# Kernel tuning notes

Measured on AMD Instinct MI355X. Metric: run time of the kernel, lower is better.

The kernel has to match this reference:

```python
import jax, jax.numpy as jnp
import numpy as np


def setup_inputs() -> dict:
    key = jax.random.key(0)
    ks = jax.random.split(key, 5)
    B, S, D = 2, 2048, 1024
    inv = 1.0 / np.sqrt(D)
    inp = {
        "x": jax.random.normal(ks[0], (B, S, D), jnp.float32),
        "Wq": jax.random.normal(ks[1], (D, D), jnp.float32) * inv,
        "bq": jnp.zeros((D,), jnp.float32),
        "Wk": jax.random.normal(ks[2], (D, D), jnp.float32) * inv,
        "bk": jnp.zeros((D,), jnp.float32),
        "Wv": jax.random.normal(ks[3], (D, D), jnp.float32) * inv,
        "bv": jnp.zeros((D,), jnp.float32),
        "Wo": jax.random.normal(ks[4], (D, D), jnp.float32) * inv,
        "bo": jnp.zeros((D,), jnp.float32),
        "num_heads": 16,
        "window_size": 128,
    }
    return inp


def reference(x, Wq, bq, Wk, bk, Wv, bv, Wo, bo, num_heads, window_size):
    B, S, D = x.shape
    H = num_heads
    hd = D // H
    scale = 1.0 / np.sqrt(hd)

    def split_heads(t):  # [B,S,D] -> [B,H,S,hd]
        return t.reshape(B, S, H, hd).transpose(0, 2, 1, 3)

    q = split_heads(x @ Wq + bq)
    k = split_heads(x @ Wk + bk)
    v = split_heads(x @ Wv + bv)

    # dense scores, then sliding-window + causal mask (faithful to original)
    scores = jnp.einsum('bhqd,bhkd->bhqk', q, k) * scale  # [B,H,S,S]
    i = jnp.arange(S)[:, None]
    j = jnp.arange(S)[None, :]
    # position i attends to j in [i - window_size + 1, i]
    mask = (j <= i) & (j > i - window_size)
    scores = jnp.where(mask, scores, -jnp.inf)
    attn_weights = jax.nn.softmax(scores, axis=-1)  # dropout is identity in eval

    out = jnp.einsum('bhqk,bhkd->bhqd', attn_weights, v)  # [B,H,S,hd]
    out = out.transpose(0, 2, 1, 3).reshape(B, S, D)
    return out @ Wo + bo, attn_weights
```

## Files before the change

kernel.cpp:

```cpp
#include <hip/hip_runtime.h>
#include <cmath>

typedef __attribute__((ext_vector_type(8))) __bf16 v8bf;
typedef __attribute__((ext_vector_type(4))) float  v4f;

#define DEV static __device__ __forceinline__

DEV unsigned short f2bf(float f) {
  unsigned u = __builtin_bit_cast(unsigned, f);
  unsigned r = u + 0x7fffu + ((u >> 16) & 1u);
  return (unsigned short)(r >> 16);
}
DEV float bf2f(unsigned short s) {
  return __builtin_bit_cast(float, ((unsigned)s) << 16);
}
DEV v8bf ld8(const unsigned short* p) { return *(const v8bf*)p; }

DEV void gl16(const unsigned short* g, unsigned short* l) {
  __builtin_amdgcn_global_load_lds(
      (const __attribute__((address_space(1))) unsigned int*)g,
      (__attribute__((address_space(3))) unsigned int*)l, 16, 0, 0);
}

__global__ __launch_bounds__(256) void k_prep(const float* __restrict__ x,
                                              const float* __restrict__ Wq,
                                              const float* __restrict__ Wk,
                                              const float* __restrict__ Wv,
                                              const float* __restrict__ Wo,
                                              const float* __restrict__ bq,
                                              const float* __restrict__ bk,
                                              const float* __restrict__ bv,
                                              unsigned short* __restrict__ xb,
                                              unsigned short* __restrict__ WT,
                                              unsigned short* __restrict__ WoT,
                                              float* __restrict__ bqkv) {
  __shared__ float t[32][33];
  int bx = blockIdx.x, tid = threadIdx.x;
  if (bx < 4096) {
    int i = bx * 256 + tid;
    float4 v = ((const float4*)x)[i];
    unsigned lo = (unsigned)f2bf(v.x) | ((unsigned)f2bf(v.y) << 16);
    unsigned hi = (unsigned)f2bf(v.z) | ((unsigned)f2bf(v.w) << 16);
    ((uint2*)xb)[i] = make_uint2(lo, hi);
  } else if (bx < 8192) {
    int rem = bx - 4096;
    int z = rem >> 10, r2 = rem & 1023;
    const float* src = (z == 0) ? Wq : (z == 1) ? Wk : (z == 2) ? Wv : Wo;
    unsigned short* dst = (z < 3) ? WT + z * 1048576 : WoT;
    int n0 = (r2 & 31) * 32, k0 = (r2 >> 5) * 32;
    int tx = tid & 31, ty = tid >> 5;
    for (int r = ty; r < 32; r += 8)
      t[r][tx] = src[(k0 + r) * 1024 + n0 + tx];
    __syncthreads();
    for (int r = ty; r < 32; r += 8)
      dst[(n0 + r) * 1024 + k0 + tx] = f2bf(t[tx][r]);
  } else {
    int i = (bx - 8192) * 256 + tid;
    float v = (i < 1024) ? bq[i] : (i < 2048 ? bk[i - 1024] : bv[i - 2048]);
    bqkv[i] = v;
  }
}

__global__ __launch_bounds__(256) void k_gemm1(const unsigned short* __restrict__ A,
                                               const unsigned short* __restrict__ Bt,
                                               const float* __restrict__ bias,
                                               unsigned short* __restrict__ Cout,
                                               unsigned short* __restrict__ Vtg) {
  constexpr int K = 1024;
  __shared__ __attribute__((aligned(16))) unsigned short As[128 * 32];
  __shared__ __attribute__((aligned(16))) unsigned short Bs[128 * 32];
  int tid = threadIdx.x;
  int wave = tid >> 6, lane = tid & 63;
  int m0 = blockIdx.y * 128, n0 = blockIdx.x * 128;
  int wm = (wave >> 1) * 64, wn = (wave & 1) * 64;
  int m = lane & 15, q4 = lane >> 4;
  int arow = tid >> 2, acol = (tid & 3) * 8;
  v4f acc[4][4] = {};
  const unsigned short* ga0 = A + (m0 + arow) * K + acol;
  const unsigned short* ga1 = A + (m0 + 64 + arow) * K + acol;
  const unsigned short* gb0 = Bt + (n0 + arow) * K + acol;
  const unsigned short* gb1 = Bt + (n0 + 64 + arow) * K + acol;
  unsigned short* lA0 = As + wave * 512;
  unsigned short* lA1 = As + 2048 + wave * 512;
  unsigned short* lB0 = Bs + wave * 512;
  unsigned short* lB1 = Bs + 2048 + wave * 512;

  for (int kt = 0; kt < K; kt += 32) {
    gl16(ga0 + kt, lA0);
    gl16(ga1 + kt, lA1);
    gl16(gb0 + kt, lB0);
    gl16(gb1 + kt, lB1);
    __syncthreads();
    v8bf af[4], bfv[4];
#pragma unroll
    for (int mt = 0; mt < 4; mt++) af[mt] = ld8(&As[(wm + mt * 16 + m) * 32 + q4 * 8]);
#pragma unroll
    for (int nt = 0; nt < 4; nt++) bfv[nt] = ld8(&Bs[(wn + nt * 16 + m) * 32 + q4 * 8]);
#pragma unroll
    for (int mt = 0; mt < 4; mt++)
#pragma unroll
      for (int nt = 0; nt < 4; nt++)
        acc[mt][nt] = __builtin_amdgcn_mfma_f32_16x16x32_bf16(af[mt], bfv[nt], acc[mt][nt], 0, 0, 0);
    __syncthreads();
  }
  if (n0 < 2048) {
#pragma unroll
    for (int mt = 0; mt < 4; mt++)
#pragma unroll
      for (int nt = 0; nt < 4; nt++) {
        int col = n0 + wn + nt * 16 + m;
        float bb = bias[col];
#pragma unroll
        for (int r = 0; r < 4; r++) {
          int row = m0 + wm + mt * 16 + q4 * 4 + r;
          Cout[row * 3072 + col] = f2bf(acc[mt][nt][r] + bb);
        }
      }
  } else {
    int b = m0 >> 11;
#pragma unroll
    for (int mt = 0; mt < 4; mt++)
#pragma unroll
      for (int nt = 0; nt < 4; nt++) {
        int col = n0 + wn + nt * 16 + m;
        float bb = bias[col];
        int dfull = col - 2048;
        int s = (m0 & 2047) + wm + mt * 16 + q4 * 4;
        unsigned short e0 = f2bf(acc[mt][nt][0] + bb);
        unsigned short e1 = f2bf(acc[mt][nt][1] + bb);
        unsigned short e2 = f2bf(acc[mt][nt][2] + bb);
        unsigned short e3 = f2bf(acc[mt][nt][3] + bb);
        uint2 pk = make_uint2((unsigned)e0 | ((unsigned)e1 << 16),
                              (unsigned)e2 | ((unsigned)e3 << 16));
        *(uint2*)&Vtg[((size_t)(b * 1024 + dfull)) * 2048 + s] = pk;
      }
  }
}

__global__ __launch_bounds__(256, 4) void k_attn(const unsigned short* __restrict__ QKV,
                                                 const unsigned short* __restrict__ Vtg,
                                                 unsigned short* __restrict__ Oatt,
                                                 unsigned short* __restrict__ cb) {
  constexpr int PSS = 168;
  __shared__ __attribute__((aligned(16))) unsigned short Ps[4][16 * PSS];
  int b = blockIdx.z, h = blockIdx.y, i0 = blockIdx.x * 64;
  int tid = threadIdx.x, wave = tid >> 6, lane = tid & 63;
  int kbase = i0 - 128;
  const int ld = 3072;
  const unsigned short* Qg = QKV + b * 2048 * ld + h * 64;
  const unsigned short* Kg = Qg + 1024;
  const unsigned short* vsrc = Vtg + (size_t)(b * 16 + h) * 64 * 2048;

  for (int c = lane; c < 16 * 24; c += 64)
    Ps[wave][(c / 24) * PSS + 144 + (c % 24)] = 0;

  int qb = i0 + wave * 16;
  int m = lane & 15, q4 = lane >> 4;

  const unsigned short* qrow = Qg + (qb + m) * ld;
  v8bf qa0 = ld8(qrow + q4 * 8);
  v8bf qa1 = ld8(qrow + 32 + q4 * 8);

  v4f sc[9];
#pragma unroll
  for (int n = 0; n < 9; n++) {
    int key = kbase + wave * 16 + n * 16 + m;
    int kg = key < 0 ? 0 : key;
    const unsigned short* krow = Kg + kg * ld;
    v8bf kb0 = ld8(krow + q4 * 8);
    v8bf kb1 = ld8(krow + 32 + q4 * 8);
    v4f z = {0.f, 0.f, 0.f, 0.f};
    z = __builtin_amdgcn_mfma_f32_16x16x32_bf16(qa0, kb0, z, 0, 0, 0);
    z = __builtin_amdgcn_mfma_f32_16x16x32_bf16(qa1, kb1, z, 0, 0, 0);
    sc[n] = z;
  }
  float mx[4] = {-3e38f, -3e38f, -3e38f, -3e38f};
#pragma unroll
  for (int n = 0; n < 9; n++)
#pragma unroll
    for (int r = 0; r < 4; r++) {
      int i = qb + q4 * 4 + r;
      int j = kbase + wave * 16 + n * 16 + m;
      float v = sc[n][r] * 0.125f;
      bool ok = (j >= 0) && (j <= i) && (j > i - 128);
      v = ok ? v : -3e38f;
      sc[n][r] = v;
      mx[r] = fmaxf(mx[r], v);
    }
#pragma unroll
  for (int o = 1; o < 16; o <<= 1)
#pragma unroll
    for (int r = 0; r < 4; r++) mx[r] = fmaxf(mx[r], __shfl_xor(mx[r], o, 64));
  float sum[4] = {0.f, 0.f, 0.f, 0.f};
#pragma unroll
  for (int n = 0; n < 9; n++)
#pragma unroll
    for (int r = 0; r < 4; r++) {
      float p = __expf(sc[n][r] - mx[r]);
      sc[n][r] = p;
      sum[r] += p;
    }
#pragma unroll
  for (int o = 1; o < 16; o <<= 1)
#pragma unroll
    for (int r = 0; r < 4; r++) sum[r] += __shfl_xor(sum[r], o, 64);
  float inv[4];
#pragma unroll
  for (int r = 0; r < 4; r++) inv[r] = 1.0f / sum[r];

#pragma unroll
  for (int n = 0; n < 9; n++)
#pragma unroll
    for (int r = 0; r < 4; r++)
      Ps[wave][(q4 * 4 + r) * PSS + n * 16 + m] = f2bf(sc[n][r] * inv[r]);

  v4f oacc[4] = {};
#pragma unroll
  for (int c = 0; c < 5; c++) {
    v8bf pa = ld8(&Ps[wave][m * PSS + c * 32 + q4 * 8]);
    int vcol = kbase + wave * 16 + c * 32 + q4 * 8;
    vcol = vcol < 0 ? 0 : (vcol > 2040 ? 2040 : vcol);
#pragma unroll
    for (int dt = 0; dt < 4; dt++) {
      v8bf vb = ld8(vsrc + (size_t)(dt * 16 + m) * 2048 + vcol);
      oacc[dt] = __builtin_amdgcn_mfma_f32_16x16x32_bf16(pa, vb, oacc[dt], 0, 0, 0);
    }
  }
#pragma unroll
  for (int dt = 0; dt < 4; dt++)
#pragma unroll
    for (int r = 0; r < 4; r++)
      Oatt[(b * 2048 + qb + q4 * 4 + r) * 1024 + h * 64 + dt * 16 + m] = f2bf(oacc[dt][r]);

  for (int R = 0; R < 16; R++) {
    int row = (b * 16 + h) * 2048 + qb + R;
    unsigned short p0 = Ps[wave][R * PSS + R + 1 + lane * 2];
    unsigned short p1 = Ps[wave][R * PSS + R + 2 + lane * 2];
    ((unsigned*)cb)[row * 64 + lane] = (unsigned)p0 | ((unsigned)p1 << 16);
  }
}

__global__ __launch_bounds__(256) void k_tail(const unsigned short* __restrict__ Oat,
                                              const unsigned short* __restrict__ WoT,
                                              const float* __restrict__ bo,
                                              float* __restrict__ out,
                                              const unsigned short* __restrict__ cb,
                                              float* __restrict__ wout) {
  __shared__ __attribute__((aligned(16))) unsigned short As[128 * 32];
  __shared__ __attribute__((aligned(16))) unsigned short Bs[128 * 32];
  int tid = threadIdx.x, wave = tid >> 6, lane = tid & 63;

  if (blockIdx.x < 256) {
    constexpr int K = 1024;
    int bx = blockIdx.x;
    int n0 = (bx & 7) * 128, m0 = (bx >> 3) * 128;
    int wm = (wave >> 1) * 64, wn = (wave & 1) * 64;
    int m = lane & 15, q4 = lane >> 4;
    int arow = tid >> 2, acol = (tid & 3) * 8;
    v4f acc[4][4] = {};
    const unsigned short* ga0 = Oat + (m0 + arow) * K + acol;
    const unsigned short* ga1 = Oat + (m0 + 64 + arow) * K + acol;
    const unsigned short* gb0 = WoT + (n0 + arow) * K + acol;
    const unsigned short* gb1 = WoT + (n0 + 64 + arow) * K + acol;
    unsigned short* lA0 = As + wave * 512;
    unsigned short* lA1 = As + 2048 + wave * 512;
    unsigned short* lB0 = Bs + wave * 512;
    unsigned short* lB1 = Bs + 2048 + wave * 512;
    for (int kt = 0; kt < K; kt += 32) {
      gl16(ga0 + kt, lA0);
      gl16(ga1 + kt, lA1);
      gl16(gb0 + kt, lB0);
      gl16(gb1 + kt, lB1);
      __syncthreads();
      v8bf af[4], bfv[4];
#pragma unroll
      for (int mt = 0; mt < 4; mt++) af[mt] = ld8(&As[(wm + mt * 16 + m) * 32 + q4 * 8]);
#pragma unroll
      for (int nt = 0; nt < 4; nt++) bfv[nt] = ld8(&Bs[(wn + nt * 16 + m) * 32 + q4 * 8]);
#pragma unroll
      for (int mt = 0; mt < 4; mt++)
#pragma unroll
        for (int nt = 0; nt < 4; nt++)
          acc[mt][nt] = __builtin_amdgcn_mfma_f32_16x16x32_bf16(af[mt], bfv[nt], acc[mt][nt], 0, 0, 0);
      __syncthreads();
    }
#pragma unroll
    for (int mt = 0; mt < 4; mt++)
#pragma unroll
      for (int nt = 0; nt < 4; nt++) {
        int col = n0 + wn + nt * 16 + m;
        float bb = bo[col];
#pragma unroll
        for (int r = 0; r < 4; r++) {
          int row = m0 + wm + mt * 16 + q4 * 4 + r;
          out[row * 1024 + col] = acc[mt][nt][r] + bb;
        }
      }
  } else {
    int wb = blockIdx.x - 256;
    int rbase = wb * 16 + wave * 4;
    for (int rr = 0; rr < 4; rr++) {
      int row = rbase + rr;
      int i = row & 2047;
      float* rowp = wout + (size_t)row * 2048;
      const unsigned short* crow = cb + (size_t)row * 128;
      int lo = i - 127;
#pragma unroll
      for (int it = 0; it < 8; it++) {
        int col = it * 256 + lane * 4;
        v4f v = {0.f, 0.f, 0.f, 0.f};
        if (col <= i && col + 3 >= lo) {
#pragma unroll
          for (int e = 0; e < 4; e++) {
            int j = col + e;
            if (j >= lo && j <= i && j >= 0)
              v[e] = bf2f(crow[j - lo]);
          }
        }
        __builtin_nontemporal_store(v, (v4f*)(rowp + col));
      }
    }
  }
}

extern "C" void kernel_launch(void* const* d_in, const int* in_sizes, int n_in,
                              void* d_out, int out_size, void* d_ws, size_t ws_size,
                              hipStream_t stream) {
  (void)in_sizes; (void)n_in; (void)out_size; (void)ws_size;
  const float* x  = (const float*)d_in[0];
  const float* Wq = (const float*)d_in[1];
  const float* bq = (const float*)d_in[2];
  const float* Wk = (const float*)d_in[3];
  const float* bk = (const float*)d_in[4];
  const float* Wv = (const float*)d_in[5];
  const float* bv = (const float*)d_in[6];
  const float* Wo = (const float*)d_in[7];
  const float* bo = (const float*)d_in[8];

  char* ws = (char*)d_ws;
  unsigned short* xb   = (unsigned short*)(ws);
  unsigned short* WT   = (unsigned short*)(ws + 8388608);
  unsigned short* WoT  = (unsigned short*)(ws + 14680064);
  float*          bqkv = (float*)(ws + 16777216);
  unsigned short* QKV  = (unsigned short*)(ws + 16789504);
  unsigned short* Oat  = (unsigned short*)(ws + 41955328);
  unsigned short* cb   = (unsigned short*)(ws + 50343936);
  unsigned short* Vtg  = (unsigned short*)(ws + 67121152);

  float* out  = (float*)d_out;
  float* wout = out + 4194304;

  k_prep<<<8204, 256, 0, stream>>>(x, Wq, Wk, Wv, Wo, bq, bk, bv, xb, WT, WoT, bqkv);
  k_gemm1<<<dim3(24, 32), 256, 0, stream>>>(xb, WT, bqkv, QKV, Vtg);
  k_attn<<<dim3(32, 16, 2), 256, 0, stream>>>(QKV, Vtg, Oat, cb);
  k_tail<<<4352, 256, 0, stream>>>(Oat, WoT, bo, out, cb, wout);
}
```

Measured before the change: 650.2 us.

## Overlap attention-weight zero fill with GEMM and attention kernels

After: 662.8 us. No clear change (+1.9%).

```diff
diff --git a/kernel.cpp b/kernel.cpp
--- a/kernel.cpp
+++ b/kernel.cpp
@@ -65,13 +65,23 @@
                                                const unsigned short* __restrict__ Bt,
                                                const float* __restrict__ bias,
                                                unsigned short* __restrict__ Cout,
-                                               unsigned short* __restrict__ Vtg) {
+                                               unsigned short* __restrict__ Vtg,
+                                               float* __restrict__ wout) {
+  int bx = blockIdx.x, tid = threadIdx.x;
+  if (bx % 3 != 0) {
+    int z = bx - bx / 3 - 1;
+    v4f zv = {0.f, 0.f, 0.f, 0.f};
+    v4f* w4 = (v4f*)wout;
+    for (size_t idx = (size_t)z * 256 + tid; idx < 16777216u; idx += 1536u * 256u)
+      __builtin_nontemporal_store(zv, w4 + idx);
+    return;
+  }
+  int g = bx / 3;
   constexpr int K = 1024;
   __shared__ __attribute__((aligned(16))) unsigned short As[128 * 32];
   __shared__ __attribute__((aligned(16))) unsigned short Bs[128 * 32];
-  int tid = threadIdx.x;
   int wave = tid >> 6, lane = tid & 63;
-  int m0 = blockIdx.y * 128, n0 = blockIdx.x * 128;
+  int m0 = (g / 24) * 128, n0 = (g % 24) * 128;
   int wm = (wave >> 1) * 64, wn = (wave & 1) * 64;
   int m = lane & 15, q4 = lane >> 4;
   int arow = tid >> 2, acol = (tid & 3) * 8;
@@ -140,11 +150,22 @@
 __global__ __launch_bounds__(256, 4) void k_attn(const unsigned short* __restrict__ QKV,
                                                  const unsigned short* __restrict__ Vtg,
                                                  unsigned short* __restrict__ Oatt,
-                                                 unsigned short* __restrict__ cb) {
+                                                 unsigned short* __restrict__ cb,
+                                                 float* __restrict__ wout) {
   constexpr int PSS = 168;
   __shared__ __attribute__((aligned(16))) unsigned short Ps[4][16 * PSS];
-  int b = blockIdx.z, h = blockIdx.y, i0 = blockIdx.x * 64;
-  int tid = threadIdx.x, wave = tid >> 6, lane = tid & 63;
+  int bx = blockIdx.x, tid = threadIdx.x;
+  if (bx & 1) {
+    int z = bx >> 1;
+    v4f zv = {0.f, 0.f, 0.f, 0.f};
+    v4f* w4 = (v4f*)wout + 16777216u;
+    for (size_t idx = (size_t)z * 256 + tid; idx < 16777216u; idx += 1024u * 256u)
+      __builtin_nontemporal_store(zv, w4 + idx);
+    return;
+  }
+  int id = bx >> 1;
+  int b = id >> 9, h = (id >> 5) & 15, i0 = (id & 31) * 64;
+  int wave = tid >> 6, lane = tid & 63;
   int kbase = i0 - 128;
   const int ld = 3072;
   const unsigned short* Qg = QKV + b * 2048 * ld + h * 64;
@@ -297,28 +318,17 @@
         }
       }
   } else {
-    int wb = blockIdx.x - 256;
-    int rbase = wb * 16 + wave * 4;
-    for (int rr = 0; rr < 4; rr++) {
+    int id = blockIdx.x - 256;
+    int rbase = id * 64 + wave * 16;
+    for (int rr = 0; rr < 16; rr++) {
       int row = rbase + rr;
       int i = row & 2047;
+      int lo = i - 127; if (lo < 0) lo = 0;
+      const unsigned short* crow = cb + (size_t)row * 128;
       float* rowp = wout + (size_t)row * 2048;
-      const unsigned short* crow = cb + (size_t)row * 128;
-      int lo = i - 127;
-#pragma unroll
-      for (int it = 0; it < 8; it++) {
-        int col = it * 256 + lane * 4;
-        v4f v = {0.f, 0.f, 0.f, 0.f};
-        if (col <= i && col + 3 >= lo) {
-#pragma unroll
-          for (int e = 0; e < 4; e++) {
-            int j = col + e;
-            if (j >= lo && j <= i && j >= 0)
-              v[e] = bf2f(crow[j - lo]);
-          }
-        }
-        __builtin_nontemporal_store(v, (v4f*)(rowp + col));
-      }
+      int c0 = lo + lane * 2;
+      if (c0 <= i)     rowp[c0]     = bf2f(crow[c0 - i + 127]);
+      if (c0 + 1 <= i) rowp[c0 + 1] = bf2f(crow[c0 + 1 - i + 127]);
     }
   }
 }
@@ -351,7 +361,7 @@
   float* wout = out + 4194304;
 
   k_prep<<<8204, 256, 0, stream>>>(x, Wq, Wk, Wv, Wo, bq, bk, bv, xb, WT, WoT, bqkv);
-  k_gemm1<<<dim3(24, 32), 256, 0, stream>>>(xb, WT, bqkv, QKV, Vtg);
-  k_attn<<<dim3(32, 16, 2), 256, 0, stream>>>(QKV, Vtg, Oat, cb);
-  k_tail<<<4352, 256, 0, stream>>>(Oat, WoT, bo, out, cb, wout);
-}
+  k_gemm1<<<2304, 256, 0, stream>>>(xb, WT, bqkv, QKV, Vtg, wout);
+  k_attn<<<2048, 256, 0, stream>>>(QKV, Vtg, Oat, cb, wout);
+  k_tail<<<1280, 256, 0, stream>>>(Oat, WoT, bo, out, cb, wout);
+}
```
